# Kernel optimization log

Measured on AMD Instinct MI355X. Metric: run time of the kernel, lower is better.

The kernel has to match this reference:

```python
import jax, jax.numpy as jnp
import numpy as np

N = 50000   # nodes
E = 800000  # edges (avg degree 16)
D = 128     # in_channels == out_channels == edge_dim
BN_EPS = 1e-5
LN_EPS = 1e-5


def setup_inputs() -> dict:
    key = jax.random.key(0)
    ks = jax.random.split(key, 8)
    s = 0.05
    return {
        "x": jax.random.normal(ks[0], (N, D), jnp.float32),
        "edge_index": jax.random.randint(ks[1], (2, E), 0, N, dtype=jnp.int64),
        "edge_attr": jax.random.normal(ks[2], (E, D), jnp.float32),
        "eps": jnp.zeros((), jnp.float32),                       # GINE train_eps init 0
        "We": jax.random.normal(ks[3], (D, D), jnp.float32) * s,  # edge lin: edge_dim -> in_channels
        "be": jnp.zeros((D,), jnp.float32),
        "W1": jax.random.normal(ks[4], (D, D), jnp.float32) * s,  # mlp first linear
        "b1": jnp.zeros((D,), jnp.float32),
        "bn_g": jnp.ones((D,), jnp.float32),
        "bn_b": jnp.zeros((D,), jnp.float32),
        "bn_rm": jnp.zeros((D,), jnp.float32),  # running mean (eval mode)
        "bn_rv": jnp.ones((D,), jnp.float32),   # running var (eval mode)
        "W2": jax.random.normal(ks[5], (D, D), jnp.float32) * s,  # mlp second linear
        "b2": jnp.zeros((D,), jnp.float32),
        "ln_g": jnp.ones((D,), jnp.float32),
        "ln_b": jnp.zeros((D,), jnp.float32),
    }


def reference(x, edge_index, edge_attr, eps, We, be, W1, b1,
              bn_g, bn_b, bn_rm, bn_rv, W2, b2, ln_g, ln_b):
    src, dst = edge_index[0], edge_index[1]  # PyG: message from x_j = x[src], aggregate at dst
    # GINE message: relu(x_j + Lin(edge_attr)); gather + elementwise
    msg = jax.nn.relu(x[src] + edge_attr @ We.T + be)            # [E, D]
    aggr = jax.ops.segment_sum(msg, dst, num_segments=N)         # scatter-sum -> [N, D]
    h = (1.0 + eps) * x + aggr
    # MLP: Linear -> BatchNorm1d (eval) -> ReLU -> (Dropout=id) -> Linear
    h = h @ W1.T + b1
    h = (h - bn_rm) * jax.lax.rsqrt(bn_rv + BN_EPS) * bn_g + bn_b
    h = jax.nn.relu(h)
    h = h @ W2.T + b2
    # LayerNorm over feature dim
    mu = jnp.mean(h, axis=-1, keepdims=True)
    var = jnp.mean(jnp.square(h - mu), axis=-1, keepdims=True)
    h = (h - mu) * jax.lax.rsqrt(var + LN_EPS) * ln_g + ln_b
    # residual (Identity since in==out) + relu; dropout is identity in eval
    return jax.nn.relu(h + x)
```

## Files before the change

### kernel.cpp

```cpp
#include <hip/hip_runtime.h>
#include <hip/hip_bf16.h>

#define D 128
#define LDK 136

typedef __bf16 bf16x8 __attribute__((ext_vector_type(8)));
typedef float  f32x4  __attribute__((ext_vector_type(4)));
typedef unsigned int u32x4 __attribute__((ext_vector_type(4)));
typedef unsigned short u16;

__device__ __forceinline__ u16 f2bf(float f) {
    unsigned int u = __builtin_bit_cast(unsigned int, f);
    u = u + 0x7FFFu + ((u >> 16) & 1u);
    return (u16)(u >> 16);
}
__device__ __forceinline__ float bf2f(u16 h) {
    unsigned int u = ((unsigned int)h) << 16;
    return __builtin_bit_cast(float, u);
}
__device__ __forceinline__ unsigned int pk2(float lo, float hi) {
    return (unsigned int)f2bf(lo) | ((unsigned int)f2bf(hi) << 16);
}
__device__ __forceinline__ void cvt_store8(u16* dst, float4 a, float4 b) {
    uint4 v;
    v.x = pk2(a.x, a.y); v.y = pk2(a.z, a.w);
    v.z = pk2(b.x, b.y); v.w = pk2(b.z, b.w);
    *reinterpret_cast<uint4*>(dst) = v;
}
__device__ __forceinline__ bf16x8 cvt8r(f32x4 a, f32x4 b) {
    u32x4 v;
    v.x = pk2(a.x, a.y); v.y = pk2(a.z, a.w);
    v.z = pk2(b.x, b.y); v.w = pk2(b.z, b.w);
    return __builtin_bit_cast(bf16x8, v);
}

__global__ __launch_bounds__(256)
void xcvt_kernel(const float* __restrict__ x, u16* __restrict__ xbf, int total8) {
    int i = blockIdx.x * 256 + threadIdx.x;
    if (i < total8) {
        const f32x4* g = reinterpret_cast<const f32x4*>(x + (size_t)i * 8);
        f32x4 a = g[0], b = g[1];
        u32x4 v;
        v.x = pk2(a.x, a.y); v.y = pk2(a.z, a.w);
        v.z = pk2(b.x, b.y); v.w = pk2(b.z, b.w);
        *reinterpret_cast<u32x4*>(xbf + (size_t)i * 8) = v;
    }
}

__global__ __launch_bounds__(256)
void hist_kernel(const int* __restrict__ ei, int* __restrict__ counts, int E) {
    int e = blockIdx.x * 256 + threadIdx.x;
    if (e < E) atomicAdd(&counts[ei[E + e]], 1);
}
__global__ __launch_bounds__(256)
void scan_partial(const int* __restrict__ counts, int* __restrict__ bsum) {
    const int b = blockIdx.x, t = threadIdx.x;
    const int4 v = reinterpret_cast<const int4*>(counts + (size_t)b * 1024)[t];
    int s = v.x + v.y + v.z + v.w;
    #pragma unroll
    for (int off = 1; off < 64; off <<= 1) s += __shfl_xor(s, off);
    __shared__ int ws[4];
    if ((t & 63) == 0) ws[t >> 6] = s;
    __syncthreads();
    if (t == 0) bsum[b] = ws[0] + ws[1] + ws[2] + ws[3];
}
__global__ __launch_bounds__(256)
void scan_bsum(int* __restrict__ bsum, int nb) {
    const int t = threadIdx.x;
    int s = (t < nb) ? bsum[t] : 0;
    int inc = s;
    const int lane = t & 63;
    #pragma unroll
    for (int off = 1; off < 64; off <<= 1) {
        int v = __shfl_up(inc, off);
        if (lane >= off) inc += v;
    }
    __shared__ int ws[4];
    if (lane == 63) ws[t >> 6] = inc;
    __syncthreads();
    int woff = 0;
    for (int i = 0; i < (t >> 6); ++i) woff += ws[i];
    if (t < nb) bsum[t] = woff + inc - s;
}
__global__ __launch_bounds__(256)
void scan_emit(const int* __restrict__ counts, const int* __restrict__ bsum,
               int* __restrict__ offsets) {
    const int b = blockIdx.x, t = threadIdx.x;
    const int4 v = reinterpret_cast<const int4*>(counts + (size_t)b * 1024)[t];
    const int s = v.x + v.y + v.z + v.w;
    int inc = s;
    const int lane = t & 63;
    #pragma unroll
    for (int off = 1; off < 64; off <<= 1) {
        int u = __shfl_up(inc, off);
        if (lane >= off) inc += u;
    }
    __shared__ int ws[4];
    if (lane == 63) ws[t >> 6] = inc;
    __syncthreads();
    int woff = bsum[b];
    for (int i = 0; i < (t >> 6); ++i) woff += ws[i];
    int e0 = woff + inc - s;
    int4 o;
    o.x = e0; o.y = e0 + v.x; o.z = o.y + v.y; o.w = o.z + v.z;
    reinterpret_cast<int4*>(offsets + (size_t)b * 1024)[t] = o;
}
__global__ __launch_bounds__(256)
void scatter_kernel(const int* __restrict__ ei, int* __restrict__ off,
                    int4* __restrict__ rec, int E) {
    int e = blockIdx.x * 256 + threadIdx.x;
    if (e < E) {
        int s = ei[e];
        int d = ei[E + e];
        int p = atomicAdd(&off[d], 1);
        rec[p] = make_int4(e, s, d, 0);
    }
}

__global__ __launch_bounds__(256, 2)
void gine_edge_pers(const u16* __restrict__ xbf,
                    const float* __restrict__ ea,
                    const float* __restrict__ We,
                    const float* __restrict__ be,
                    const int4* __restrict__ rec,
                    float* __restrict__ aggr,
                    int E, int ntiles)
{
    __shared__ u16 wbuf[128][LDK];
    __shared__ u16 mbuf[128][LDK];
    __shared__ int eid_lds[128];
    __shared__ int src_lds[128];
    __shared__ int dst_lds[128];

    const int tid = threadIdx.x;
    const int wave = tid >> 6, lane = tid & 63;
    const int lhi = lane >> 4, llo = lane & 15;
    const int r0 = wave * 32;

    {
        const int row = tid >> 1;
        const int c0  = (tid & 1) * 64;
        const float4* gw = reinterpret_cast<const float4*>(We + (size_t)row * D + c0);
        #pragma unroll
        for (int j = 0; j < 8; ++j) {
            float4 w0 = gw[2*j], w1 = gw[2*j+1];
            cvt_store8(&wbuf[row][c0 + 8*j], w0, w1);
        }
    }
    float bev[8];
    #pragma unroll
    for (int nf = 0; nf < 8; ++nf) bev[nf] = be[nf*16 + llo];
    __syncthreads();

    const int xrow = tid >> 1;
    const int xc0  = (tid & 1) * 64;

    for (int tile = blockIdx.x; tile < ntiles; tile += gridDim.x) {
        const int e0 = tile * 128;

        if (tid < 128) {
            const int p = e0 + tid;
            if (p < E) {
                int4 r4 = rec[p];
                eid_lds[tid] = r4.x; src_lds[tid] = r4.y; dst_lds[tid] = r4.z;
            } else {
                eid_lds[tid] = 0; src_lds[tid] = 0; dst_lds[tid] = -1;
            }
        }
        __syncthreads();

        f32x4 acc[2][8];
        #pragma unroll
        for (int m = 0; m < 2; ++m)
            #pragma unroll
            for (int n = 0; n < 8; ++n) acc[m][n] = (f32x4){0.f, 0.f, 0.f, 0.f};

        const f32x4* pa = reinterpret_cast<const f32x4*>(ea + (size_t)eid_lds[r0 + llo] * D);
        const f32x4* pb = reinterpret_cast<const f32x4*>(ea + (size_t)eid_lds[r0 + 16 + llo] * D);
        const u32x4* gx = reinterpret_cast<const u32x4*>(xbf + (size_t)src_lds[xrow] * D + xc0);

#define LOADG(G, KK) { const int f4_ = ((KK)*32 + lhi*8) >> 2;                 \
        G[0] = __builtin_nontemporal_load(pa + f4_);                           \
        G[1] = __builtin_nontemporal_load(pa + f4_ + 1);                       \
        G[2] = __builtin_nontemporal_load(pb + f4_);                           \
        G[3] = __builtin_nontemporal_load(pb + f4_ + 1); }
#define MFMAG(G, KK) { bf16x8 a0_ = cvt8r(G[0], G[1]);                         \
        bf16x8 a1_ = cvt8r(G[2], G[3]);                                        \
        const int k0_ = (KK)*32 + lhi*8;                                       \
        _Pragma("unroll")                                                      \
        for (int nf = 0; nf < 8; ++nf) {                                       \
            bf16x8 b_ = *reinterpret_cast<const bf16x8*>(&wbuf[nf*16 + llo][k0_]); \
            acc[0][nf] = __builtin_amdgcn_mfma_f32_16x16x32_bf16(a0_, b_, acc[0][nf], 0, 0, 0); \
            acc[1][nf] = __builtin_amdgcn_mfma_f32_16x16x32_bf16(a1_, b_, acc[1][nf], 0, 0, 0); \
        } }

        f32x4 gA[4], gB[4];
        u32x4 xa[8];
        LOADG(gA, 0); LOADG(gB, 1);
        #pragma unroll
        for (int j = 0; j < 8; ++j) xa[j] = gx[j];
        MFMAG(gA, 0); LOADG(gA, 2);
        MFMAG(gB, 1); LOADG(gB, 3);
        MFMAG(gA, 2); MFMAG(gB, 3);
#undef LOADG
#undef MFMAG

        #pragma unroll
        for (int j = 0; j < 8; ++j)
            *reinterpret_cast<u32x4*>(&mbuf[xrow][xc0 + 8*j]) = xa[j];

        #pragma unroll
        for (int mf = 0; mf < 2; ++mf) {
            #pragma unroll
            for (int r = 0; r < 4; ++r) {
                const int row = r0 + mf*16 + lhi*4 + r;
                const bool valid = (e0 + row) < E;
                #pragma unroll
                for (int nf = 0; nf < 8; ++nf) {
                    const int col = nf*16 + llo;
                    const float v = acc[mf][nf][r] + bf2f(mbuf[row][col]) + bev[nf];
                    mbuf[row][col] = valid ? f2bf(fmaxf(v, 0.0f)) : (u16)0;
                }
            }
        }
        __syncthreads();

        {
            const int c   = tid & 127;
            const int h   = tid >> 7;
            const int rlo = h * 64;
            float sum = 0.0f;
            int prev  = dst_lds[rlo];
            int start = rlo;
            #pragma unroll 4
            for (int r = rlo; r < rlo + 64; ++r) {
                const float v = bf2f(mbuf[r][c]);
                const int d = dst_lds[r];
                if (d != prev) {
                    if (prev >= 0) {
                        float* p = &aggr[(size_t)prev * D + c];
                        if (start == rlo) atomicAdd(p, sum);
                        else              *p = sum;
                    }
                    sum = 0.0f; prev = d; start = r;
                }
                sum += v;
            }
            if (prev >= 0) atomicAdd(&aggr[(size_t)prev * D + c], sum);
        }
        __syncthreads();
    }
}

__global__ __launch_bounds__(256, 4)
void gine_edge(const float* __restrict__ x,
               const int* __restrict__ ei,
               const float* __restrict__ ea,
               const float* __restrict__ We,
               const float* __restrict__ be,
               float* __restrict__ aggr,
               int E)
{
    __shared__ u16 w_lds[128][LDK];
    __shared__ int sd_lds[2][128];

    const int tid = threadIdx.x;
    const int e0  = blockIdx.x * 128;

    {
        const int row = tid >> 1;
        const int c0  = (tid & 1) * 64;
        const float4* gw = reinterpret_cast<const float4*>(We + (size_t)row * D + c0);
        #pragma unroll
        for (int j = 0; j < 8; ++j) {
            float4 w0 = gw[2*j], w1 = gw[2*j+1];
            cvt_store8(&w_lds[row][c0 + 8*j], w0, w1);
        }
        const int r = tid & 127, which = tid >> 7;
        int erow = e0 + r;
        sd_lds[which][r] = (erow < E) ? ei[(size_t)which * E + erow] : 0;
    }
    __syncthreads();

    const int wave = tid >> 6, lane = tid & 63;
    const int lhi = lane >> 4, llo = lane & 15;
    const int r0 = wave * 32;

    f32x4 acc[2][8];
    #pragma unroll
    for (int m = 0; m < 2; ++m)
        #pragma unroll
        for (int n = 0; n < 8; ++n) acc[m][n] = (f32x4){0.f, 0.f, 0.f, 0.f};

    int ra = e0 + r0 + llo;      if (ra >= E) ra = E - 1;
    int rb = e0 + r0 + 16 + llo; if (rb >= E) rb = E - 1;
    const f32x4* pa = reinterpret_cast<const f32x4*>(ea + (size_t)ra * D);
    const f32x4* pb = reinterpret_cast<const f32x4*>(ea + (size_t)rb * D);

    #pragma unroll
    for (int kk = 0; kk < 4; ++kk) {
        const int k0 = kk * 32 + lhi * 8;
        const int f4 = k0 >> 2;
        f32x4 u0 = __builtin_nontemporal_load(pa + f4);
        f32x4 u1 = __builtin_nontemporal_load(pa + f4 + 1);
        f32x4 v0 = __builtin_nontemporal_load(pb + f4);
        f32x4 v1 = __builtin_nontemporal_load(pb + f4 + 1);
        bf16x8 a0 = cvt8r(u0, u1);
        bf16x8 a1 = cvt8r(v0, v1);
        #pragma unroll
        for (int nf = 0; nf < 8; ++nf) {
            bf16x8 b = *reinterpret_cast<const bf16x8*>(&w_lds[nf*16 + llo][k0]);
            acc[0][nf] = __builtin_amdgcn_mfma_f32_16x16x32_bf16(a0, b, acc[0][nf], 0, 0, 0);
            acc[1][nf] = __builtin_amdgcn_mfma_f32_16x16x32_bf16(a1, b, acc[1][nf], 0, 0, 0);
        }
    }

    float bev[8];
    #pragma unroll
    for (int nf = 0; nf < 8; ++nf) bev[nf] = be[nf*16 + llo];

    #pragma unroll
    for (int mf = 0; mf < 2; ++mf) {
        #pragma unroll
        for (int r = 0; r < 4; ++r) {
            const int row = r0 + mf*16 + lhi*4 + r;
            if (e0 + row >= E) continue;
            const int s = sd_lds[0][row];
            const int d = sd_lds[1][row];
            const float* xr  = x    + (size_t)s * D;
            float*      arow = aggr + (size_t)d * D;
            #pragma unroll
            for (int nf = 0; nf < 8; ++nf) {
                const int col = nf*16 + llo;
                float v = acc[mf][nf][r] + xr[col] + bev[nf];
                atomicAdd(&arow[col], fmaxf(v, 0.0f));
            }
        }
    }
}

__global__ __launch_bounds__(256, 2)
void gine_node(const float* __restrict__ x,
               const float* __restrict__ aggr,
               const float* __restrict__ epsp,
               const float* __restrict__ W1,
               const float* __restrict__ b1,
               const float* __restrict__ bn_g,
               const float* __restrict__ bn_b,
               const float* __restrict__ bn_rm,
               const float* __restrict__ bn_rv,
               const float* __restrict__ W2,
               const float* __restrict__ b2,
               const float* __restrict__ ln_g,
               const float* __restrict__ ln_b,
               float* __restrict__ out,
               int N)
{
    __shared__ u16 h_lds[128][LDK];
    __shared__ u16 w_lds[128][LDK];

    const int tid = threadIdx.x;
    const int n0  = blockIdx.x * 128;
    const float epf = 1.0f + epsp[0];

    {
        const int row = tid >> 1;
        const int c0  = (tid & 1) * 64;
        int nrow = n0 + row; if (nrow >= N) nrow = N - 1;
        const float4* gx = reinterpret_cast<const float4*>(x    + (size_t)nrow * D + c0);
        const float4* ga = reinterpret_cast<const float4*>(aggr + (size_t)nrow * D + c0);
        const float4* gw = reinterpret_cast<const float4*>(W1   + (size_t)row  * D + c0);
        #pragma unroll
        for (int j = 0; j < 8; ++j) {
            float4 xv0 = gx[2*j], xv1 = gx[2*j+1];
            float4 av0 = ga[2*j], av1 = ga[2*j+1];
            float4 h0, h1;
            h0.x = epf*xv0.x + av0.x; h0.y = epf*xv0.y + av0.y;
            h0.z = epf*xv0.z + av0.z; h0.w = epf*xv0.w + av0.w;
            h1.x = epf*xv1.x + av1.x; h1.y = epf*xv1.y + av1.y;
            h1.z = epf*xv1.z + av1.z; h1.w = epf*xv1.w + av1.w;
            cvt_store8(&h_lds[row][c0 + 8*j], h0, h1);
            float4 w0 = gw[2*j], w1 = gw[2*j+1];
            cvt_store8(&w_lds[row][c0 + 8*j], w0, w1);
        }
    }
    __syncthreads();

    const int wave = tid >> 6, lane = tid & 63;
    const int lhi = lane >> 4, llo = lane & 15;
    const int r0 = wave * 32;

    f32x4 acc[2][8];
    #pragma unroll
    for (int m = 0; m < 2; ++m)
        #pragma unroll
        for (int n = 0; n < 8; ++n) acc[m][n] = (f32x4){0.f, 0.f, 0.f, 0.f};

    #pragma unroll
    for (int kk = 0; kk < 4; ++kk) {
        const int k0 = kk * 32 + lhi * 8;
        bf16x8 a0 = *reinterpret_cast<const bf16x8*>(&h_lds[r0 + llo][k0]);
        bf16x8 a1 = *reinterpret_cast<const bf16x8*>(&h_lds[r0 + 16 + llo][k0]);
        #pragma unroll
        for (int nf = 0; nf < 8; ++nf) {
            bf16x8 b = *reinterpret_cast<const bf16x8*>(&w_lds[nf*16 + llo][k0]);
            acc[0][nf] = __builtin_amdgcn_mfma_f32_16x16x32_bf16(a0, b, acc[0][nf], 0, 0, 0);
            acc[1][nf] = __builtin_amdgcn_mfma_f32_16x16x32_bf16(a1, b, acc[1][nf], 0, 0, 0);
        }
    }

    float sc[8], bi[8], b2v[8], lgv[8], lbv[8];
    #pragma unroll
    for (int nf = 0; nf < 8; ++nf) {
        const int c = nf*16 + llo;
        const float s = bn_g[c] * rsqrtf(bn_rv[c] + 1e-5f);
        sc[nf]  = s;
        bi[nf]  = (b1[c] - bn_rm[c]) * s + bn_b[c];
        b2v[nf] = b2[c];
        lgv[nf] = ln_g[c];
        lbv[nf] = ln_b[c];
    }

    __syncthreads();

    #pragma unroll
    for (int mf = 0; mf < 2; ++mf) {
        #pragma unroll
        for (int r = 0; r < 4; ++r) {
            const int row = r0 + mf*16 + lhi*4 + r;
            #pragma unroll
            for (int nf = 0; nf < 8; ++nf) {
                const int col = nf*16 + llo;
                const float v = fmaxf(acc[mf][nf][r] * sc[nf] + bi[nf], 0.0f);
                h_lds[row][col] = f2bf(v);
            }
        }
    }
    {
        const int row = tid >> 1;
        const int c0  = (tid & 1) * 64;
        const float4* gw = reinterpret_cast<const float4*>(W2 + (size_t)row * D + c0);
        #pragma unroll
        for (int j = 0; j < 8; ++j) {
            float4 w0 = gw[2*j], w1 = gw[2*j+1];
            cvt_store8(&w_lds[row][c0 + 8*j], w0, w1);
        }
    }
    __syncthreads();

    f32x4 acc2[2][8];
    #pragma unroll
    for (int m = 0; m < 2; ++m)
        #pragma unroll
        for (int n = 0; n < 8; ++n) acc2[m][n] = (f32x4){0.f, 0.f, 0.f, 0.f};

    #pragma unroll
    for (int kk = 0; kk < 4; ++kk) {
        const int k0 = kk * 32 + lhi * 8;
        bf16x8 a0 = *reinterpret_cast<const bf16x8*>(&h_lds[r0 + llo][k0]);
        bf16x8 a1 = *reinterpret_cast<const bf16x8*>(&h_lds[r0 + 16 + llo][k0]);
        #pragma unroll
        for (int nf = 0; nf < 8; ++nf) {
            bf16x8 b = *reinterpret_cast<const bf16x8*>(&w_lds[nf*16 + llo][k0]);
            acc2[0][nf] = __builtin_amdgcn_mfma_f32_16x16x32_bf16(a0, b, acc2[0][nf], 0, 0, 0);
            acc2[1][nf] = __builtin_amdgcn_mfma_f32_16x16x32_bf16(a1, b, acc2[1][nf], 0, 0, 0);
        }
    }

    #pragma unroll
    for (int mf = 0; mf < 2; ++mf) {
        #pragma unroll
        for (int r = 0; r < 4; ++r) {
            float hv[8];
            float ssum = 0.f;
            #pragma unroll
            for (int nf = 0; nf < 8; ++nf) {
                const float v = acc2[mf][nf][r] + b2v[nf];
                hv[nf] = v; ssum += v;
            }
            ssum += __shfl_xor(ssum, 1); ssum += __shfl_xor(ssum, 2);
            ssum += __shfl_xor(ssum, 4); ssum += __shfl_xor(ssum, 8);
            const float mu = ssum * (1.0f/128.0f);
            float qs = 0.f;
            #pragma unroll
            for (int nf = 0; nf < 8; ++nf) { const float dd = hv[nf] - mu; qs += dd*dd; }
            qs += __shfl_xor(qs, 1); qs += __shfl_xor(qs, 2);
            qs += __shfl_xor(qs, 4); qs += __shfl_xor(qs, 8);
            const float rstd = rsqrtf(qs * (1.0f/128.0f) + 1e-5f);

            const int nrow = n0 + r0 + mf*16 + lhi*4 + r;
            if (nrow < N) {
                const float* xr   = x   + (size_t)nrow * D;
                float*       orow = out + (size_t)nrow * D;
                #pragma unroll
                for (int nf = 0; nf < 8; ++nf) {
                    const int col = nf*16 + llo;
                    const float v = (hv[nf] - mu) * rstd * lgv[nf] + lbv[nf] + xr[col];
                    orow[col] = fmaxf(v, 0.0f);
                }
            }
        }
    }
}

extern "C" void kernel_launch(void* const* d_in, const int* in_sizes, int n_in,
                              void* d_out, int out_size, void* d_ws, size_t ws_size,
                              hipStream_t stream) {
    const float* x     = (const float*)d_in[0];
    const int*   ei    = (const int*)d_in[1];
    const float* ea    = (const float*)d_in[2];
    const float* epsp  = (const float*)d_in[3];
    const float* We    = (const float*)d_in[4];
    const float* be    = (const float*)d_in[5];
    const float* W1    = (const float*)d_in[6];
    const float* b1    = (const float*)d_in[7];
    const float* bn_g  = (const float*)d_in[8];
    const float* bn_b  = (const float*)d_in[9];
    const float* bn_rm = (const float*)d_in[10];
    const float* bn_rv = (const float*)d_in[11];
    const float* W2    = (const float*)d_in[12];
    const float* b2    = (const float*)d_in[13];
    const float* ln_g  = (const float*)d_in[14];
    const float* ln_b  = (const float*)d_in[15];
    float* out = (float*)d_out;

    const int N = in_sizes[0] / D;
    const int E = in_sizes[2] / D;

    const size_t aggr_bytes = (size_t)N * D * sizeof(float);
    const size_t cnt_elems  = ((size_t)N + 1023) & ~(size_t)1023;
    const size_t cnt_bytes  = cnt_elems * sizeof(int);
    const size_t bsum_bytes = 1024;
    const size_t rec4_bytes = (size_t)E * sizeof(int4);
    const size_t xbf_bytes  = (size_t)N * D * sizeof(u16);
    const size_t base       = aggr_bytes + 2 * cnt_bytes + bsum_bytes;
    const size_t need_mid   = base + rec4_bytes + xbf_bytes;
    const int nsb = (int)(cnt_elems / 1024);

    char* wsb = (char*)d_ws;
    const int tblocks = (E + 255) / 256;
    const int eblocks = (E + 127) / 128;
    const int nblocks = (N + 127) / 128;
    const int ntiles  = (E + 127) / 128;
    const int pblocks = (ntiles < 512) ? ntiles : 512;
    const int total8  = N * D / 8;
    const int xblocks = (total8 + 255) / 256;

    if (ws_size >= need_mid && nsb <= 256) {
        float* aggr    = (float*)(wsb);
        int*   counts  = (int*)(wsb + aggr_bytes);
        int*   offsets = (int*)(wsb + aggr_bytes + cnt_bytes);
        int*   bsum    = (int*)(wsb + aggr_bytes + 2*cnt_bytes);
        int4*  rec     = (int4*)(wsb + base);
        u16*   xbf     = (u16*)(wsb + base + rec4_bytes);

        (void)hipMemsetAsync(aggr, 0, aggr_bytes, stream);
        (void)hipMemsetAsync(counts, 0, cnt_bytes, stream);

        xcvt_kernel<<<xblocks, 256, 0, stream>>>(x, xbf, total8);
        hist_kernel<<<tblocks, 256, 0, stream>>>(ei, counts, E);
        scan_partial<<<nsb, 256, 0, stream>>>(counts, bsum);
        scan_bsum<<<1, 256, 0, stream>>>(bsum, nsb);
        scan_emit<<<nsb, 256, 0, stream>>>(counts, bsum, offsets);
        scatter_kernel<<<tblocks, 256, 0, stream>>>(ei, offsets, rec, E);

        gine_edge_pers<<<pblocks, 256, 0, stream>>>(xbf, ea, We, be, rec, aggr, E, ntiles);
        gine_node<<<nblocks, 256, 0, stream>>>(x, aggr, epsp, W1, b1, bn_g, bn_b,
                                               bn_rm, bn_rv, W2, b2, ln_g, ln_b, out, N);
    } else {
        float* aggr = (ws_size >= aggr_bytes) ? (float*)d_ws : out;
        (void)hipMemsetAsync(aggr, 0, aggr_bytes, stream);
        gine_edge<<<eblocks, 256, 0, stream>>>(x, ei, ea, We, be, aggr, E);
        gine_node<<<nblocks, 256, 0, stream>>>(x, aggr, epsp, W1, b1, bn_g, bn_b,
                                               bn_rm, bn_rv, W2, b2, ln_g, ln_b, out, N);
    }
}
```

Before: 341.4 us.

## Prefetch next edge tile's gathers during scatter, pack edge records, merge prep kernels

The persistent edge kernel now double-buffers the per-tile edge id, source and destination arrays. It issues the next tile's edge_attr and x gathers into registers before doing the current tile's segmented scatter-add, so global load latency overlaps the atomic reduction phase. Edge records shrink from int4 to a packed 64-bit word, which cuts record traffic, and the x-to-bf16 conversion and histogram kernels are merged into one launch. In exchange, register pressure rises because the full tile of gathered data is held across iterations, and packing only applies when E and N fit the bit fields, with a fallback path otherwise.

```diff
diff --git a/kernel.cpp b/kernel.cpp
--- a/kernel.cpp
+++ b/kernel.cpp
@@ -8,6 +8,7 @@
 typedef float  f32x4  __attribute__((ext_vector_type(4)));
 typedef unsigned int u32x4 __attribute__((ext_vector_type(4)));
 typedef unsigned short u16;
+typedef unsigned long long u64;
 
 __device__ __forceinline__ u16 f2bf(float f) {
     unsigned int u = __builtin_bit_cast(unsigned int, f);
@@ -35,23 +36,26 @@
 }
 
 __global__ __launch_bounds__(256)
-void xcvt_kernel(const float* __restrict__ x, u16* __restrict__ xbf, int total8) {
-    int i = blockIdx.x * 256 + threadIdx.x;
-    if (i < total8) {
-        const f32x4* g = reinterpret_cast<const f32x4*>(x + (size_t)i * 8);
-        f32x4 a = g[0], b = g[1];
-        u32x4 v;
-        v.x = pk2(a.x, a.y); v.y = pk2(a.z, a.w);
-        v.z = pk2(b.x, b.y); v.w = pk2(b.z, b.w);
-        *reinterpret_cast<u32x4*>(xbf + (size_t)i * 8) = v;
-    }
-}
-
-__global__ __launch_bounds__(256)
-void hist_kernel(const int* __restrict__ ei, int* __restrict__ counts, int E) {
-    int e = blockIdx.x * 256 + threadIdx.x;
-    if (e < E) atomicAdd(&counts[ei[E + e]], 1);
-}
+void pre_kernel(const float* __restrict__ x, u16* __restrict__ xbf, int total8,
+                const int* __restrict__ ei, int* __restrict__ counts, int E,
+                int xblocks) {
+    const int b = blockIdx.x;
+    if (b < xblocks) {
+        int i = b * 256 + threadIdx.x;
+        if (i < total8) {
+            const f32x4* g = reinterpret_cast<const f32x4*>(x + (size_t)i * 8);
+            f32x4 a = g[0], c = g[1];
+            u32x4 v;
+            v.x = pk2(a.x, a.y); v.y = pk2(a.z, a.w);
+            v.z = pk2(c.x, c.y); v.w = pk2(c.z, c.w);
+            *reinterpret_cast<u32x4*>(xbf + (size_t)i * 8) = v;
+        }
+    } else {
+        int e = (b - xblocks) * 256 + threadIdx.x;
+        if (e < E) atomicAdd(&counts[ei[E + e]], 1);
+    }
+}
+
 __global__ __launch_bounds__(256)
 void scan_partial(const int* __restrict__ counts, int* __restrict__ bsum) {
     const int b = blockIdx.x, t = threadIdx.x;
@@ -105,15 +109,16 @@
     o.x = e0; o.y = e0 + v.x; o.z = o.y + v.y; o.w = o.z + v.z;
     reinterpret_cast<int4*>(offsets + (size_t)b * 1024)[t] = o;
 }
+
 __global__ __launch_bounds__(256)
 void scatter_kernel(const int* __restrict__ ei, int* __restrict__ off,
-                    int4* __restrict__ rec, int E) {
+                    u64* __restrict__ rec, int E) {
     int e = blockIdx.x * 256 + threadIdx.x;
     if (e < E) {
-        int s = ei[e];
-        int d = ei[E + e];
-        int p = atomicAdd(&off[d], 1);
-        rec[p] = make_int4(e, s, d, 0);
+        u64 s = (u64)ei[e];
+        u64 d = (u64)ei[E + e];
+        int p = atomicAdd(&off[(int)d], 1);
+        rec[p] = (u64)e | (s << 20) | (d << 37);
     }
 }
 
@@ -122,20 +127,22 @@
                     const float* __restrict__ ea,
                     const float* __restrict__ We,
                     const float* __restrict__ be,
-                    const int4* __restrict__ rec,
+                    const u64* __restrict__ rec,
                     float* __restrict__ aggr,
                     int E, int ntiles)
 {
     __shared__ u16 wbuf[128][LDK];
     __shared__ u16 mbuf[128][LDK];
-    __shared__ int eid_lds[128];
-    __shared__ int src_lds[128];
-    __shared__ int dst_lds[128];
+    __shared__ int eid_lds[2][128];
+    __shared__ int src_lds[2][128];
+    __shared__ int dst_lds[2][128];
 
     const int tid = threadIdx.x;
     const int wave = tid >> 6, lane = tid & 63;
     const int lhi = lane >> 4, llo = lane & 15;
     const int r0 = wave * 32;
+    const int xrow = tid >> 1;
+    const int xc0  = (tid & 1) * 64;
 
     {
         const int row = tid >> 1;
@@ -150,60 +157,78 @@
     float bev[8];
     #pragma unroll
     for (int nf = 0; nf < 8; ++nf) bev[nf] = be[nf*16 + llo];
-    __syncthreads();
-
-    const int xrow = tid >> 1;
-    const int xc0  = (tid & 1) * 64;
+
+    if (tid < 128) {
+        const int p = blockIdx.x * 128 + tid;
+        if (p < E) {
+            u64 v = rec[p];
+            eid_lds[0][tid] = (int)(v & 0xFFFFFu);
+            src_lds[0][tid] = (int)((v >> 20) & 0x1FFFFu);
+            dst_lds[0][tid] = (int)(v >> 37);
+        } else {
+            eid_lds[0][tid] = 0; src_lds[0][tid] = 0; dst_lds[0][tid] = -1;
+        }
+    }
+    __syncthreads();
+
+    f32x4 ga[16];
+    u32x4 xa[8];
+
+#define ISSUE(BUF) {                                                            \
+        const f32x4* pa_ = reinterpret_cast<const f32x4*>(                      \
+            ea + (size_t)eid_lds[BUF][r0 + llo] * D);                           \
+        const f32x4* pb_ = reinterpret_cast<const f32x4*>(                      \
+            ea + (size_t)eid_lds[BUF][r0 + 16 + llo] * D);                      \
+        const u32x4* gx_ = reinterpret_cast<const u32x4*>(                      \
+            xbf + (size_t)src_lds[BUF][xrow] * D + xc0);                        \
+        _Pragma("unroll")                                                       \
+        for (int kk = 0; kk < 4; ++kk) {                                        \
+            const int f4_ = (kk*32 + lhi*8) >> 2;                               \
+            ga[kk*4+0] = __builtin_nontemporal_load(pa_ + f4_);                 \
+            ga[kk*4+1] = __builtin_nontemporal_load(pa_ + f4_ + 1);             \
+            ga[kk*4+2] = __builtin_nontemporal_load(pb_ + f4_);                 \
+            ga[kk*4+3] = __builtin_nontemporal_load(pb_ + f4_ + 1);             \
+        }                                                                       \
+        _Pragma("unroll")                                                       \
+        for (int j = 0; j < 8; ++j) xa[j] = gx_[j]; }
+
+    ISSUE(0);
+    int cur = 0;
 
     for (int tile = blockIdx.x; tile < ntiles; tile += gridDim.x) {
-        const int e0 = tile * 128;
-
-        if (tid < 128) {
-            const int p = e0 + tid;
+        const int e0  = tile * 128;
+        const int nxt = tile + gridDim.x;
+
+        if (tid < 128 && nxt < ntiles) {
+            const int p = nxt * 128 + tid;
             if (p < E) {
-                int4 r4 = rec[p];
-                eid_lds[tid] = r4.x; src_lds[tid] = r4.y; dst_lds[tid] = r4.z;
+                u64 v = rec[p];
+                eid_lds[cur^1][tid] = (int)(v & 0xFFFFFu);
+                src_lds[cur^1][tid] = (int)((v >> 20) & 0x1FFFFu);
+                dst_lds[cur^1][tid] = (int)(v >> 37);
             } else {
-                eid_lds[tid] = 0; src_lds[tid] = 0; dst_lds[tid] = -1;
-            }
-        }
-        __syncthreads();
+                eid_lds[cur^1][tid] = 0; src_lds[cur^1][tid] = 0;
+                dst_lds[cur^1][tid] = -1;
+            }
+        }
 
         f32x4 acc[2][8];
         #pragma unroll
         for (int m = 0; m < 2; ++m)
             #pragma unroll
             for (int n = 0; n < 8; ++n) acc[m][n] = (f32x4){0.f, 0.f, 0.f, 0.f};
-
-        const f32x4* pa = reinterpret_cast<const f32x4*>(ea + (size_t)eid_lds[r0 + llo] * D);
-        const f32x4* pb = reinterpret_cast<const f32x4*>(ea + (size_t)eid_lds[r0 + 16 + llo] * D);
-        const u32x4* gx = reinterpret_cast<const u32x4*>(xbf + (size_t)src_lds[xrow] * D + xc0);
-
-#define LOADG(G, KK) { const int f4_ = ((KK)*32 + lhi*8) >> 2;                 \
-        G[0] = __builtin_nontemporal_load(pa + f4_);                           \
-        G[1] = __builtin_nontemporal_load(pa + f4_ + 1);                       \
-        G[2] = __builtin_nontemporal_load(pb + f4_);                           \
-        G[3] = __builtin_nontemporal_load(pb + f4_ + 1); }
-#define MFMAG(G, KK) { bf16x8 a0_ = cvt8r(G[0], G[1]);                         \
-        bf16x8 a1_ = cvt8r(G[2], G[3]);                                        \
-        const int k0_ = (KK)*32 + lhi*8;                                       \
-        _Pragma("unroll")                                                      \
-        for (int nf = 0; nf < 8; ++nf) {                                       \
-            bf16x8 b_ = *reinterpret_cast<const bf16x8*>(&wbuf[nf*16 + llo][k0_]); \
-            acc[0][nf] = __builtin_amdgcn_mfma_f32_16x16x32_bf16(a0_, b_, acc[0][nf], 0, 0, 0); \
-            acc[1][nf] = __builtin_amdgcn_mfma_f32_16x16x32_bf16(a1_, b_, acc[1][nf], 0, 0, 0); \
-        } }
-
-        f32x4 gA[4], gB[4];
-        u32x4 xa[8];
-        LOADG(gA, 0); LOADG(gB, 1);
-        #pragma unroll
-        for (int j = 0; j < 8; ++j) xa[j] = gx[j];
-        MFMAG(gA, 0); LOADG(gA, 2);
-        MFMAG(gB, 1); LOADG(gB, 3);
-        MFMAG(gA, 2); MFMAG(gB, 3);
-#undef LOADG
-#undef MFMAG
+        #pragma unroll
+        for (int kk = 0; kk < 4; ++kk) {
+            bf16x8 a0 = cvt8r(ga[kk*4+0], ga[kk*4+1]);
+            bf16x8 a1 = cvt8r(ga[kk*4+2], ga[kk*4+3]);
+            const int k0 = kk*32 + lhi*8;
+            #pragma unroll
+            for (int nf = 0; nf < 8; ++nf) {
+                bf16x8 b = *reinterpret_cast<const bf16x8*>(&wbuf[nf*16 + llo][k0]);
+                acc[0][nf] = __builtin_amdgcn_mfma_f32_16x16x32_bf16(a0, b, acc[0][nf], 0, 0, 0);
+                acc[1][nf] = __builtin_amdgcn_mfma_f32_16x16x32_bf16(a1, b, acc[1][nf], 0, 0, 0);
+            }
+        }
 
         #pragma unroll
         for (int j = 0; j < 8; ++j)
@@ -225,17 +250,19 @@
         }
         __syncthreads();
 
+        if (nxt < ntiles) ISSUE(cur^1);
+
         {
             const int c   = tid & 127;
             const int h   = tid >> 7;
             const int rlo = h * 64;
             float sum = 0.0f;
-            int prev  = dst_lds[rlo];
+            int prev  = dst_lds[cur][rlo];
             int start = rlo;
             #pragma unroll 4
             for (int r = rlo; r < rlo + 64; ++r) {
                 const float v = bf2f(mbuf[r][c]);
-                const int d = dst_lds[r];
+                const int d = dst_lds[cur][r];
                 if (d != prev) {
                     if (prev >= 0) {
                         float* p = &aggr[(size_t)prev * D + c];
@@ -248,8 +275,13 @@
             }
             if (prev >= 0) atomicAdd(&aggr[(size_t)prev * D + c], sum);
         }
-        __syncthreads();
-    }
+
+        asm volatile("s_waitcnt lgkmcnt(0)" ::: "memory");
+        __builtin_amdgcn_s_barrier();
+        asm volatile("" ::: "memory");
+        cur ^= 1;
+    }
+#undef ISSUE
 }
 
 __global__ __launch_bounds__(256, 4)
@@ -531,11 +563,12 @@
     const size_t cnt_elems  = ((size_t)N + 1023) & ~(size_t)1023;
     const size_t cnt_bytes  = cnt_elems * sizeof(int);
     const size_t bsum_bytes = 1024;
-    const size_t rec4_bytes = (size_t)E * sizeof(int4);
+    const size_t rec8_bytes = (size_t)E * sizeof(u64);
     const size_t xbf_bytes  = (size_t)N * D * sizeof(u16);
     const size_t base       = aggr_bytes + 2 * cnt_bytes + bsum_bytes;
-    const size_t need_mid   = base + rec4_bytes + xbf_bytes;
+    const size_t need_mid   = base + rec8_bytes + xbf_bytes;
     const int nsb = (int)(cnt_elems / 1024);
+    const bool packable = (E < (1 << 20)) && (N < (1 << 17));
 
     char* wsb = (char*)d_ws;
     const int tblocks = (E + 255) / 256;
@@ -546,19 +579,18 @@
     const int total8  = N * D / 8;
     const int xblocks = (total8 + 255) / 256;
 
-    if (ws_size >= need_mid && nsb <= 256) {
+    if (ws_size >= need_mid && nsb <= 256 && packable) {
         float* aggr    = (float*)(wsb);
         int*   counts  = (int*)(wsb + aggr_bytes);
         int*   offsets = (int*)(wsb + aggr_bytes + cnt_bytes);
         int*   bsum    = (int*)(wsb + aggr_bytes + 2*cnt_bytes);
-        int4*  rec     = (int4*)(wsb + base);
-        u16*   xbf     = (u16*)(wsb + base + rec4_bytes);
+        u64*   rec     = (u64*)(wsb + base);
+        u16*   xbf     = (u16*)(wsb + base + rec8_bytes);
 
         (void)hipMemsetAsync(aggr, 0, aggr_bytes, stream);
         (void)hipMemsetAsync(counts, 0, cnt_bytes, stream);
 
-        xcvt_kernel<<<xblocks, 256, 0, stream>>>(x, xbf, total8);
-        hist_kernel<<<tblocks, 256, 0, stream>>>(ei, counts, E);
+        pre_kernel<<<xblocks + tblocks, 256, 0, stream>>>(x, xbf, total8, ei, counts, E, xblocks);
         scan_partial<<<nsb, 256, 0, stream>>>(counts, bsum);
         scan_bsum<<<1, 256, 0, stream>>>(bsum, nsb);
         scan_emit<<<nsb, 256, 0, stream>>>(counts, bsum, offsets);
```

New measurement: 348.0 us. No clear change (+1.9%).
